# Kernel optimization log

Measured on AMD Instinct MI355X. Metric: run time of the kernel, lower is better.

Reference implementation:

```python
import jax, jax.numpy as jnp
import numpy as np

NUM_HEADS = 8
NUM_GROUPS = 8
EPS = 1e-5


def group_norm(x, scale, bias):
    # x: [B, C, H, W]; GroupNorm with NUM_GROUPS groups, per-channel affine.
    B, C, H, W = x.shape
    xg = x.reshape(B, NUM_GROUPS, C // NUM_GROUPS, H, W)
    mean = jnp.mean(xg, axis=(2, 3, 4), keepdims=True)
    var = jnp.var(xg, axis=(2, 3, 4), keepdims=True)
    xg = (xg - mean) * jax.lax.rsqrt(var + EPS)
    xn = xg.reshape(B, C, H, W)
    return xn * scale[None, :, None, None] + bias[None, :, None, None]


def setup_inputs() -> dict:
    key = jax.random.key(0)
    ks = jax.random.split(key, 4)
    B, C, H, W = 8, 256, 32, 32
    x = jax.random.normal(ks[0], (B, C, H, W), dtype=jnp.float32)
    gn_scale = jnp.ones((C,), dtype=jnp.float32)
    gn_bias = jnp.zeros((C,), dtype=jnp.float32)
    w_qkv = jax.random.normal(ks[1], (3 * C, C), dtype=jnp.float32) * (1.0 / np.sqrt(C))
    b_qkv = jnp.zeros((3 * C,), dtype=jnp.float32)
    w_out = jax.random.normal(ks[2], (C, C), dtype=jnp.float32) * (1.0 / np.sqrt(C))
    b_out = jnp.zeros((C,), dtype=jnp.float32)
    return {"x": x, "gn_scale": gn_scale, "gn_bias": gn_bias,
            "w_qkv": w_qkv, "b_qkv": b_qkv, "w_out": w_out, "b_out": b_out}


def reference(x, gn_scale, gn_bias, w_qkv, b_qkv, w_out, b_out):
    B, C, H, W = x.shape
    hd = C // NUM_HEADS  # head_dim
    N = H * W

    h = group_norm(x, gn_scale, gn_bias)
    # 1x1 conv == channel matmul: [B, 3C, H, W]
    qkv = jnp.einsum('oc,bchw->bohw', w_qkv, h) + b_qkv[None, :, None, None]
    q, k, v = jnp.split(qkv, 3, axis=1)
    # [B, heads, head_dim, N]
    q = q.reshape(B, NUM_HEADS, hd, N)
    k = k.reshape(B, NUM_HEADS, hd, N)
    v = v.reshape(B, NUM_HEADS, hd, N)

    scale = 1.0 / np.sqrt(hd).astype(np.float32)
    attn = jnp.einsum('bhdn,bhdm->bhnm', q, k) * scale  # [B, h, N, N]
    attn = jax.nn.softmax(attn, axis=-1)
    out = jnp.einsum('bhnm,bhdm->bhdn', attn, v)  # [B, h, hd, N]
    out = out.reshape(B, C, H, W)
    out = jnp.einsum('oc,bchw->bohw', w_out, out) + b_out[None, :, None, None]
    return x + out
```

## Files before the change

kernel.cpp:

```cpp
#include <hip/hip_runtime.h>
#include <math.h>

#define BB 8
#define CC 256
#define NN 1024
#define HEADS 8
#define HDIM 32
#define NGRP 8

using bf16x8 = __attribute__((ext_vector_type(8))) short;
using f32x4  = __attribute__((ext_vector_type(4))) float;

static __device__ __forceinline__ ushort f2bf(float x) {
  unsigned u = __float_as_uint(x);
  unsigned r = (u + 0x7FFFu + ((u >> 16) & 1u)) >> 16;
  return (ushort)r;
}

__global__ __launch_bounds__(256) void wcast_kernel(
    const float* __restrict__ wqkv, const float* __restrict__ wout,
    ushort* __restrict__ wbf)
{
  const int gid = blockIdx.x * 256 + threadIdx.x;
  const int e8 = gid * 8;
  const float* src = (e8 < 196608) ? (wqkv + e8) : (wout + (e8 - 196608));
  const float4 a = *(const float4*)src;
  const float4 c = *(const float4*)(src + 4);
  union { uint4 v; ushort s[8]; } o;
  o.s[0] = f2bf(a.x); o.s[1] = f2bf(a.y); o.s[2] = f2bf(a.z); o.s[3] = f2bf(a.w);
  o.s[4] = f2bf(c.x); o.s[5] = f2bf(c.y); o.s[6] = f2bf(c.z); o.s[7] = f2bf(c.w);
  *(uint4*)(wbf + e8) = o.v;
}

__global__ __launch_bounds__(1024) void gn_kernel(
    const float* __restrict__ x, const float* __restrict__ gns,
    const float* __restrict__ gnb, ushort* __restrict__ h)
{
  const int t = threadIdx.x;
  const int b = blockIdx.x >> 3, g = blockIdx.x & 7;
  const size_t base = (((size_t)b * CC + (size_t)g * 32) * NN);
  const float4* x4 = (const float4*)(x + base);
  ushort* hb = h + base;

  float4 r[8];
  float s = 0.f, ss = 0.f;
#pragma unroll
  for (int j = 0; j < 8; ++j) {
    r[j] = x4[t + j * 1024];
    s  += r[j].x + r[j].y + r[j].z + r[j].w;
    ss += r[j].x * r[j].x + r[j].y * r[j].y + r[j].z * r[j].z + r[j].w * r[j].w;
  }
#pragma unroll
  for (int off = 32; off > 0; off >>= 1) {
    s  += __shfl_down(s, off);
    ss += __shfl_down(ss, off);
  }
  __shared__ float rs[16], rss[16];
  __shared__ float smean, srstd;
  const int wid = t >> 6, lane = t & 63;
  if (lane == 0) { rs[wid] = s; rss[wid] = ss; }
  __syncthreads();
  if (t == 0) {
    float S = 0.f, SS = 0.f;
    for (int i = 0; i < 16; ++i) { S += rs[i]; SS += rss[i]; }
    const float mean = S * (1.f / 32768.f);
    const float var = SS * (1.f / 32768.f) - mean * mean;
    smean = mean;
    srstd = rsqrtf(var + 1e-5f);
  }
  __syncthreads();
  const float mean = smean, rstd = srstd;
#pragma unroll
  for (int j = 0; j < 8; ++j) {
    const int c = g * 32 + (t >> 8) + 4 * j;
    const float sc = gns[c] * rstd;
    const float bi = gnb[c];
    ushort4 w4;
    w4.x = f2bf((r[j].x - mean) * sc + bi);
    w4.y = f2bf((r[j].y - mean) * sc + bi);
    w4.z = f2bf((r[j].z - mean) * sc + bi);
    w4.w = f2bf((r[j].w - mean) * sc + bi);
    *(ushort4*)&hb[(size_t)(t + j * 1024) * 4] = w4;
  }
}

template <int MODE>
__global__ __launch_bounds__(256) void conv_mfma_kernel(
    const ushort* __restrict__ Wbf, const float* __restrict__ bias,
    const ushort* __restrict__ X, const float* __restrict__ xres,
    ushort* __restrict__ qT, ushort* __restrict__ kT, ushort* __restrict__ vN,
    float* __restrict__ out)
{
  const int t = threadIdx.x;
  const int w = t >> 6, l = t & 63;
  const int lg = l >> 4, lr = l & 15;
  const int wr = w >> 1, wc = w & 1;
  const int b = blockIdx.z;
  const int o0 = blockIdx.y << 6, n0 = blockIdx.x << 6;

  __shared__ ushort Ws[64][72];
  __shared__ ushort Xs[64][72];

  union FragU { ushort4 u[2]; bf16x8 f; };
  f32x4 acc[2][2] = {};

  const ushort* Xb = X + (size_t)b * 256 * 1024;

  for (int k0 = 0; k0 < 256; k0 += 64) {
    __syncthreads();
#pragma unroll
    for (int li = 0; li < 2; ++li) {
      const int id = t + (li << 8);
      const int rr = id >> 3, c8 = id & 7;
      const uint4 wv = *(const uint4*)(Wbf + (size_t)(o0 + rr) * 256 + k0 + c8 * 8);
      *(uint4*)&Ws[rr][c8 * 8] = wv;
      if (MODE == 1) {
        const uint4 xv = *(const uint4*)(Xb + (size_t)(n0 + rr) * 256 + k0 + c8 * 8);
        *(uint4*)&Xs[rr][c8 * 8] = xv;
      } else {
        union { uint4 v; ushort s[8]; } xv;
        xv.v = *(const uint4*)(Xb + (size_t)(k0 + rr) * 1024 + n0 + c8 * 8);
#pragma unroll
        for (int j = 0; j < 8; ++j) Xs[c8 * 8 + j][rr] = xv.s[j];
      }
    }
    __syncthreads();

    FragU af[2][2], xf[2][2];
#pragma unroll
    for (int i = 0; i < 2; ++i)
#pragma unroll
      for (int kc = 0; kc < 2; ++kc) {
        const ushort* p = &Ws[wr * 32 + i * 16 + lr][kc * 32 + lg * 4];
        af[i][kc].u[0] = *(const ushort4*)p;
        af[i][kc].u[1] = *(const ushort4*)(p + 16);
        const ushort* q = &Xs[wc * 32 + i * 16 + lr][kc * 32 + lg * 4];
        xf[i][kc].u[0] = *(const ushort4*)q;
        xf[i][kc].u[1] = *(const ushort4*)(q + 16);
      }
#pragma unroll
    for (int ms = 0; ms < 2; ++ms)
#pragma unroll
      for (int ns = 0; ns < 2; ++ns) {
        acc[ms][ns] = __builtin_amdgcn_mfma_f32_16x16x32_bf16(af[ms][0].f, xf[ns][0].f, acc[ms][ns], 0, 0, 0);
        acc[ms][ns] = __builtin_amdgcn_mfma_f32_16x16x32_bf16(af[ms][1].f, xf[ns][1].f, acc[ms][ns], 0, 0, 0);
      }
  }

  if (MODE == 0) {
    const int sec = o0 >> 8;
    const float scl = (sec == 0) ? 0.17677669529663689f : 1.0f;
#pragma unroll
    for (int ms = 0; ms < 2; ++ms) {
      const int ob = o0 + wr * 32 + ms * 16 + lg * 4;
      const float4 b4 = *(const float4*)(bias + ob);
      const int oo = ob & 255;
      const int hh = oo >> 5, d0 = oo & 31;
      const int bh = b * 8 + hh;
#pragma unroll
      for (int ns = 0; ns < 2; ++ns) {
        const int n = n0 + wc * 32 + ns * 16 + lr;
        float v0 = (acc[ms][ns][0] + b4.x) * scl;
        float v1 = (acc[ms][ns][1] + b4.y) * scl;
        float v2 = (acc[ms][ns][2] + b4.z) * scl;
        float v3 = (acc[ms][ns][3] + b4.w) * scl;
        if (sec < 2) {
          ushort* dst = (sec == 0) ? qT : kT;
          ushort4 w4 = {f2bf(v0), f2bf(v1), f2bf(v2), f2bf(v3)};
          *(ushort4*)&dst[((size_t)bh * 1024 + n) * 32 + d0] = w4;
        } else {
          vN[((size_t)bh * 32 + d0 + 0) * 1024 + n] = f2bf(v0);
          vN[((size_t)bh * 32 + d0 + 1) * 1024 + n] = f2bf(v1);
          vN[((size_t)bh * 32 + d0 + 2) * 1024 + n] = f2bf(v2);
          vN[((size_t)bh * 32 + d0 + 3) * 1024 + n] = f2bf(v3);
        }
      }
    }
  } else {
#pragma unroll
    for (int ms = 0; ms < 2; ++ms) {
      const int ob = o0 + wr * 32 + ms * 16 + lg * 4;
      const float4 b4 = *(const float4*)(bias + ob);
#pragma unroll
      for (int ns = 0; ns < 2; ++ns) {
        const int n = n0 + wc * 32 + ns * 16 + lr;
        const size_t i0 = ((size_t)b * 256 + ob) * 1024 + n;
        out[i0]          = acc[ms][ns][0] + b4.x + xres[i0];
        out[i0 + 1024]   = acc[ms][ns][1] + b4.y + xres[i0 + 1024];
        out[i0 + 2048]   = acc[ms][ns][2] + b4.z + xres[i0 + 2048];
        out[i0 + 3072]   = acc[ms][ns][3] + b4.w + xres[i0 + 3072];
      }
    }
  }
}

__global__ __launch_bounds__(256) void attn_kernel(
    const ushort* __restrict__ qT, const ushort* __restrict__ kT,
    const ushort* __restrict__ vN, ushort* __restrict__ aoT)
{
  const int t = threadIdx.x;
  const int w = t >> 6, l = t & 63;
  const int lg = l >> 4, lr = l & 15;
  const int bh = blockIdx.y;
  const int b = bh >> 3, hh = bh & 7;
  const int qbase = blockIdx.x << 6;

  __shared__ ushort Ks[64][40];
  __shared__ ushort Vs[32][72];

  union FragU { ushort4 u[2]; bf16x8 f; };

  FragU qf;
  {
    const ushort* Qp = qT + (((size_t)bh * 1024 + qbase + w * 16 + lr) * 32) + lg * 4;
    qf.u[0] = *(const ushort4*)Qp;
    qf.u[1] = *(const ushort4*)(Qp + 16);
  }

  f32x4 accO[2] = {};
  float m_st = -1e30f, l_st = 0.f;

  const ushort* Kbh = kT + (size_t)bh * 1024 * 32;
  const ushort* Vbh = vN + (size_t)bh * 32 * 1024;

  for (int m0 = 0; m0 < NN; m0 += 64) {
    __syncthreads();
    {
      const uint4 kv = ((const uint4*)(Kbh + (size_t)m0 * 32))[t];
      *(uint4*)&Ks[t >> 2][(t & 3) * 8] = kv;
      const int d = t >> 3, mq = t & 7;
      const uint4 vv = *(const uint4*)(Vbh + (size_t)d * 1024 + m0 + mq * 8);
      *(uint4*)&Vs[d][mq * 8] = vv;
    }
    __syncthreads();

    f32x4 s[4];
#pragma unroll
    for (int ms = 0; ms < 4; ++ms) {
      FragU kf;
      const ushort* kp = &Ks[ms * 16 + lr][lg * 4];
      kf.u[0] = *(const ushort4*)kp;
      kf.u[1] = *(const ushort4*)(kp + 16);
      f32x4 z = {0.f, 0.f, 0.f, 0.f};
      s[ms] = __builtin_amdgcn_mfma_f32_16x16x32_bf16(kf.f, qf.f, z, 0, 0, 0);
    }

    float mx = s[0][0];
#pragma unroll
    for (int ms = 0; ms < 4; ++ms)
#pragma unroll
      for (int r = 0; r < 4; ++r) mx = fmaxf(mx, s[ms][r]);
    mx = fmaxf(mx, __shfl_xor(mx, 16));
    mx = fmaxf(mx, __shfl_xor(mx, 32));
    const float mnew = fmaxf(m_st, mx);
    const float c = __expf(m_st - mnew);
    m_st = mnew;
    float ls = 0.f;
#pragma unroll
    for (int ms = 0; ms < 4; ++ms)
#pragma unroll
      for (int r = 0; r < 4; ++r) {
        const float p = __expf(s[ms][r] - mnew);
        s[ms][r] = p;
        ls += p;
      }
    ls += __shfl_xor(ls, 16);
    ls += __shfl_xor(ls, 32);
    l_st = l_st * c + ls;
#pragma unroll
    for (int dt = 0; dt < 2; ++dt)
#pragma unroll
      for (int r = 0; r < 4; ++r) accO[dt][r] *= c;

    bf16x8 pb[2];
#pragma unroll
    for (int mc = 0; mc < 2; ++mc) {
      bf16x8 f;
#pragma unroll
      for (int r = 0; r < 4; ++r) {
        f[r]     = (short)f2bf(s[2 * mc][r]);
        f[r + 4] = (short)f2bf(s[2 * mc + 1][r]);
      }
      pb[mc] = f;
    }

#pragma unroll
    for (int dt = 0; dt < 2; ++dt) {
#pragma unroll
      for (int mc = 0; mc < 2; ++mc) {
        FragU vf;
        const ushort* vp = &Vs[dt * 16 + lr][mc * 32 + lg * 4];
        vf.u[0] = *(const ushort4*)vp;
        vf.u[1] = *(const ushort4*)(vp + 16);
        accO[dt] = __builtin_amdgcn_mfma_f32_16x16x32_bf16(vf.f, pb[mc], accO[dt], 0, 0, 0);
      }
    }
  }

  const float inv = 1.f / l_st;
  const int n = qbase + w * 16 + lr;
  ushort* ap = aoT + ((size_t)b * 1024 + n) * 256 + hh * 32 + lg * 4;
#pragma unroll
  for (int dt = 0; dt < 2; ++dt) {
    ushort4 w4;
    w4.x = f2bf(accO[dt][0] * inv);
    w4.y = f2bf(accO[dt][1] * inv);
    w4.z = f2bf(accO[dt][2] * inv);
    w4.w = f2bf(accO[dt][3] * inv);
    *(ushort4*)(ap + dt * 16) = w4;
  }
}

extern "C" void kernel_launch(void* const* d_in, const int* in_sizes, int n_in,
                              void* d_out, int out_size, void* d_ws, size_t ws_size,
                              hipStream_t stream)
{
  const float* x    = (const float*)d_in[0];
  const float* gns  = (const float*)d_in[1];
  const float* gnb  = (const float*)d_in[2];
  const float* wqkv = (const float*)d_in[3];
  const float* bqkv = (const float*)d_in[4];
  const float* wout = (const float*)d_in[5];
  const float* bout = (const float*)d_in[6];
  float* out = (float*)d_out;

  char* ws = (char*)d_ws;
  ushort* h   = (ushort*)(ws);
  ushort* qT  = (ushort*)(ws + (4u << 20));
  ushort* kT  = (ushort*)(ws + (8u << 20));
  ushort* vN  = (ushort*)(ws + (12u << 20));
  ushort* aoT = (ushort*)(ws + (16u << 20));
  ushort* wbf = (ushort*)(ws + (20u << 20));

  wcast_kernel<<<dim3(128), dim3(256), 0, stream>>>(wqkv, wout, wbf);
  gn_kernel<<<dim3(64), dim3(1024), 0, stream>>>(x, gns, gnb, h);
  conv_mfma_kernel<0><<<dim3(16, 12, 8), dim3(256), 0, stream>>>(
      wbf, bqkv, h, nullptr, qT, kT, vN, nullptr);
  attn_kernel<<<dim3(16, 64), dim3(256), 0, stream>>>(qT, kT, vN, aoT);
  conv_mfma_kernel<1><<<dim3(16, 4, 8), dim3(256), 0, stream>>>(
      wbf + 768 * 256, bout, aoT, x, nullptr, nullptr, nullptr, out);
}
```

Before: 138.2 us.

## Widen attention KV tile, fold log2e into Q scale, pre-transpose GN output

```diff
diff --git a/kernel.cpp b/kernel.cpp
--- a/kernel.cpp
+++ b/kernel.cpp
@@ -1,4 +1,5 @@
 #include <hip/hip_runtime.h>
+#include <hip/hip_bf16.h>
 #include <math.h>
 
 #define BB 8
@@ -11,10 +12,18 @@
 using bf16x8 = __attribute__((ext_vector_type(8))) short;
 using f32x4  = __attribute__((ext_vector_type(4))) float;
 
+#if __has_builtin(__builtin_amdgcn_exp2f)
+#define EXP2(x) __builtin_amdgcn_exp2f(x)
+#else
+#define EXP2(x) exp2f(x)
+#endif
+
+#define SCL_Q_LOG2E 0.2550348892803828f
+
 static __device__ __forceinline__ ushort f2bf(float x) {
-  unsigned u = __float_as_uint(x);
-  unsigned r = (u + 0x7FFFu + ((u >> 16) & 1u)) >> 16;
-  return (ushort)r;
+  union { __hip_bfloat16 b; ushort u; } c;
+  c.b = __float2bfloat16(x);
+  return c.u;
 }
 
 __global__ __launch_bounds__(256) void wcast_kernel(
@@ -84,6 +93,36 @@
   }
 }
 
+__global__ __launch_bounds__(256) void transpose_kernel(
+    const ushort* __restrict__ h, ushort* __restrict__ hT)
+{
+  __shared__ ushort Ls[64 * 68];
+  const int t = threadIdx.x;
+  const int b = blockIdx.z;
+  const int c0 = blockIdx.y << 6, n0 = blockIdx.x << 6;
+  const ushort* hb = h + ((size_t)b * CC) * NN;
+
+#pragma unroll
+  for (int li = 0; li < 2; ++li) {
+    const int id = t + (li << 8);
+    const int cR = id >> 3, nC = id & 7;
+    union { uint4 v; ushort s[8]; } xv;
+    xv.v = *(const uint4*)(hb + (size_t)(c0 + cR) * NN + n0 + nC * 8);
+#pragma unroll
+    for (int j = 0; j < 8; ++j) Ls[(nC * 8 + j) * 68 + cR] = xv.s[j];
+  }
+  __syncthreads();
+#pragma unroll
+  for (int li = 0; li < 2; ++li) {
+    const int id = t + (li << 8);
+    const int nR = id >> 3, cP = id & 7;
+    union { uint4 v; ushort4 s[2]; } ov;
+    ov.s[0] = *(const ushort4*)&Ls[nR * 68 + cP * 8];
+    ov.s[1] = *(const ushort4*)&Ls[nR * 68 + cP * 8 + 4];
+    *(uint4*)(hT + ((size_t)b * NN + n0 + nR) * CC + c0 + cP * 8) = ov.v;
+  }
+}
+
 template <int MODE>
 __global__ __launch_bounds__(256) void conv_mfma_kernel(
     const ushort* __restrict__ Wbf, const float* __restrict__ bias,
@@ -104,7 +143,7 @@
   union FragU { ushort4 u[2]; bf16x8 f; };
   f32x4 acc[2][2] = {};
 
-  const ushort* Xb = X + (size_t)b * 256 * 1024;
+  const ushort* Xb = X + (size_t)b * 1024 * 256;
 
   for (int k0 = 0; k0 < 256; k0 += 64) {
     __syncthreads();
@@ -114,15 +153,8 @@
       const int rr = id >> 3, c8 = id & 7;
       const uint4 wv = *(const uint4*)(Wbf + (size_t)(o0 + rr) * 256 + k0 + c8 * 8);
       *(uint4*)&Ws[rr][c8 * 8] = wv;
-      if (MODE == 1) {
-        const uint4 xv = *(const uint4*)(Xb + (size_t)(n0 + rr) * 256 + k0 + c8 * 8);
-        *(uint4*)&Xs[rr][c8 * 8] = xv;
-      } else {
-        union { uint4 v; ushort s[8]; } xv;
-        xv.v = *(const uint4*)(Xb + (size_t)(k0 + rr) * 1024 + n0 + c8 * 8);
-#pragma unroll
-        for (int j = 0; j < 8; ++j) Xs[c8 * 8 + j][rr] = xv.s[j];
-      }
+      const uint4 xv = *(const uint4*)(Xb + (size_t)(n0 + rr) * 256 + k0 + c8 * 8);
+      *(uint4*)&Xs[rr][c8 * 8] = xv;
     }
     __syncthreads();
 
@@ -149,7 +181,7 @@
 
   if (MODE == 0) {
     const int sec = o0 >> 8;
-    const float scl = (sec == 0) ? 0.17677669529663689f : 1.0f;
+    const float scl = (sec == 0) ? SCL_Q_LOG2E : 1.0f;
 #pragma unroll
     for (int ms = 0; ms < 2; ++ms) {
       const int ob = o0 + wr * 32 + ms * 16 + lg * 4;
@@ -205,8 +237,8 @@
   const int b = bh >> 3, hh = bh & 7;
   const int qbase = blockIdx.x << 6;
 
-  __shared__ ushort Ks[64][40];
-  __shared__ ushort Vs[32][72];
+  __shared__ ushort Ks[128][40];
+  __shared__ ushort Vs[32][136];
 
   union FragU { ushort4 u[2]; bf16x8 f; };
 
@@ -223,20 +255,24 @@
   const ushort* Kbh = kT + (size_t)bh * 1024 * 32;
   const ushort* Vbh = vN + (size_t)bh * 32 * 1024;
 
-  for (int m0 = 0; m0 < NN; m0 += 64) {
+  for (int m0 = 0; m0 < NN; m0 += 128) {
     __syncthreads();
     {
-      const uint4 kv = ((const uint4*)(Kbh + (size_t)m0 * 32))[t];
-      *(uint4*)&Ks[t >> 2][(t & 3) * 8] = kv;
-      const int d = t >> 3, mq = t & 7;
-      const uint4 vv = *(const uint4*)(Vbh + (size_t)d * 1024 + m0 + mq * 8);
-      *(uint4*)&Vs[d][mq * 8] = vv;
+      const uint4* kp4 = (const uint4*)(Kbh + (size_t)m0 * 32);
+      const uint4 kv0 = kp4[t], kv1 = kp4[t + 256];
+      *(uint4*)&Ks[t >> 2][(t & 3) * 8] = kv0;
+      *(uint4*)&Ks[64 + (t >> 2)][(t & 3) * 8] = kv1;
+      const int d = t >> 4, m8 = (t & 15) * 8;
+      const uint4 vv0 = *(const uint4*)(Vbh + (size_t)d * 1024 + m0 + m8);
+      const uint4 vv1 = *(const uint4*)(Vbh + (size_t)(d + 16) * 1024 + m0 + m8);
+      *(uint4*)&Vs[d][m8] = vv0;
+      *(uint4*)&Vs[d + 16][m8] = vv1;
     }
     __syncthreads();
 
-    f32x4 s[4];
-#pragma unroll
-    for (int ms = 0; ms < 4; ++ms) {
+    f32x4 s[8];
+#pragma unroll
+    for (int ms = 0; ms < 8; ++ms) {
       FragU kf;
       const ushort* kp = &Ks[ms * 16 + lr][lg * 4];
       kf.u[0] = *(const ushort4*)kp;
@@ -247,20 +283,20 @@
 
     float mx = s[0][0];
 #pragma unroll
-    for (int ms = 0; ms < 4; ++ms)
+    for (int ms = 0; ms < 8; ++ms)
 #pragma unroll
       for (int r = 0; r < 4; ++r) mx = fmaxf(mx, s[ms][r]);
     mx = fmaxf(mx, __shfl_xor(mx, 16));
     mx = fmaxf(mx, __shfl_xor(mx, 32));
     const float mnew = fmaxf(m_st, mx);
-    const float c = __expf(m_st - mnew);
+    const float c = EXP2(m_st - mnew);
     m_st = mnew;
     float ls = 0.f;
 #pragma unroll
-    for (int ms = 0; ms < 4; ++ms)
+    for (int ms = 0; ms < 8; ++ms)
 #pragma unroll
       for (int r = 0; r < 4; ++r) {
-        const float p = __expf(s[ms][r] - mnew);
+        const float p = EXP2(s[ms][r] - mnew);
         s[ms][r] = p;
         ls += p;
       }
@@ -272,9 +308,9 @@
 #pragma unroll
       for (int r = 0; r < 4; ++r) accO[dt][r] *= c;
 
-    bf16x8 pb[2];
-#pragma unroll
-    for (int mc = 0; mc < 2; ++mc) {
+    bf16x8 pb[4];
+#pragma unroll
+    for (int mc = 0; mc < 4; ++mc) {
       bf16x8 f;
 #pragma unroll
       for (int r = 0; r < 4; ++r) {
@@ -287,7 +323,7 @@
 #pragma unroll
     for (int dt = 0; dt < 2; ++dt) {
 #pragma unroll
-      for (int mc = 0; mc < 2; ++mc) {
+      for (int mc = 0; mc < 4; ++mc) {
         FragU vf;
         const ushort* vp = &Vs[dt * 16 + lr][mc * 32 + lg * 4];
         vf.u[0] = *(const ushort4*)vp;
@@ -326,16 +362,18 @@
 
   char* ws = (char*)d_ws;
   ushort* h   = (ushort*)(ws);
-  ushort* qT  = (ushort*)(ws + (4u << 20));
-  ushort* kT  = (ushort*)(ws + (8u << 20));
-  ushort* vN  = (ushort*)(ws + (12u << 20));
-  ushort* aoT = (ushort*)(ws + (16u << 20));
-  ushort* wbf = (ushort*)(ws + (20u << 20));
+  ushort* hT  = (ushort*)(ws + (4u << 20));
+  ushort* qT  = (ushort*)(ws + (8u << 20));
+  ushort* kT  = (ushort*)(ws + (12u << 20));
+  ushort* vN  = (ushort*)(ws + (16u << 20));
+  ushort* aoT = (ushort*)(ws + (20u << 20));
+  ushort* wbf = (ushort*)(ws + (24u << 20));
 
   wcast_kernel<<<dim3(128), dim3(256), 0, stream>>>(wqkv, wout, wbf);
   gn_kernel<<<dim3(64), dim3(1024), 0, stream>>>(x, gns, gnb, h);
+  transpose_kernel<<<dim3(16, 4, 8), dim3(256), 0, stream>>>(h, hT);
   conv_mfma_kernel<0><<<dim3(16, 12, 8), dim3(256), 0, stream>>>(
-      wbf, bqkv, h, nullptr, qT, kT, vN, nullptr);
+      wbf, bqkv, hT, nullptr, qT, kT, vN, nullptr);
   attn_kernel<<<dim3(16, 64), dim3(256), 0, stream>>>(qT, kT, vN, aoT);
   conv_mfma_kernel<1><<<dim3(16, 4, 8), dim3(256), 0, stream>>>(
       wbf + 768 * 256, bout, aoT, x, nullptr, nullptr, nullptr, out);
```

New measurement: 127.7 us. -7.6%, faster.
